# Kernel optimization log

Measured on AMD Instinct MI355X. Metric: run time of the kernel, lower is better.

Reference implementation:

```python
import jax, jax.numpy as jnp
import numpy as np

BH, BW = 4, 4  # bin_size_h, bin_size_w
BN_EPS = 1e-5


def _patch_split(t, bh, bw):
    # b c (bh ph) (bw pw) -> b (bh bw) (ph pw) c
    b, c, h, w = t.shape
    ph, pw = h // bh, w // bw
    t = t.reshape(b, c, bh, ph, bw, pw).transpose(0, 2, 4, 3, 5, 1)
    return t.reshape(b, bh * bw, ph * pw, c)


def _patch_recover(t, bh, bw, ph, pw):
    # b (bh bw) (ph pw) c -> b c (bh ph) (bw pw)
    b, n, p, c = t.shape
    t = t.reshape(b, bh, bw, ph, pw, c).transpose(0, 5, 1, 3, 2, 4)
    return t.reshape(b, c, bh * ph, bw * pw)


def setup_inputs() -> dict:
    key = jax.random.key(0)
    ks = jax.random.split(key, 16)
    b, C, h, w = 4, 512, 128, 128      # proj_dim = 512
    mid = C // 2                        # 256
    CM = 19 * 4                         # num_classes * num_local_prototype = 76
    return {
        "x": jax.random.normal(ks[0], (b, C, h, w), jnp.float32),
        "sim_mat": jax.random.normal(ks[1], (b, CM, h, w), jnp.float32),
        "global_cls_centers": jax.random.normal(ks[2], (19, 4, C), jnp.float32),
        "Wq": jax.random.normal(ks[3], (C, mid), jnp.float32) * 0.02,
        "bq": jax.random.normal(ks[4], (mid,), jnp.float32) * 0.02,
        "Wk": jax.random.normal(ks[5], (C, mid), jnp.float32) * 0.02,
        "bk": jax.random.normal(ks[6], (mid,), jnp.float32) * 0.02,
        "Wv": jax.random.normal(ks[7], (C, mid), jnp.float32) * 0.02,
        "bv": jax.random.normal(ks[8], (mid,), jnp.float32) * 0.02,
        "Wc": jax.random.normal(ks[9], (mid, C), jnp.float32) * 0.02,
        "bn_gamma": jax.random.uniform(ks[10], (C,), jnp.float32, 0.5, 1.5),
        "bn_beta": jax.random.normal(ks[11], (C,), jnp.float32) * 0.1,
        "bn_mean": jax.random.normal(ks[12], (C,), jnp.float32) * 0.1,
        "bn_var": jax.random.uniform(ks[13], (C,), jnp.float32, 0.5, 1.5),
    }


def reference(x, sim_mat, global_cls_centers, Wq, bq, Wk, bk, Wv, bv, Wc,
              bn_gamma, bn_beta, bn_mean, bn_var):
    b, C, h, w = x.shape
    CM = sim_mat.shape[1]
    ph, pw = h // BH, w // BW

    # pool_cam: adaptive avg pool to (BH, BW) == per-patch mean
    patch_cls_score = sim_mat.reshape(b, CM, BH, ph, BW, pw).mean(axis=(3, 5))  # [b,CM,BH,BW]

    sm = _patch_split(sim_mat, BH, BW)   # [b, N, P, CM]
    xs = _patch_split(x, BH, BW)         # [b, N, P, C]

    # patch_confidence: [b, N, CM, 1]
    conf = patch_cls_score.reshape(b, CM, BH * BW).transpose(0, 2, 1)[..., None]

    sm = jax.nn.softmax(sm, axis=2)      # softmax over pixels within patch
    local = jnp.einsum('bnpc,bnpk->bnck', sm, xs) * conf  # [b, N, CM, C]

    g = global_cls_centers.reshape(CM, C)  # (c m) k

    q = xs @ Wq + bq        # [b, N, P, mid]
    k = local @ Wk + bk     # [b, N, CM, mid]
    v = g @ Wv + bv         # [CM, mid] (identical across b, n -> broadcast)

    att = jax.nn.softmax(jnp.einsum('bnpm,bncm->bnpc', q, k), axis=-1)
    out = jnp.einsum('bnpc,cm->bnpm', att, v)               # [b, N, P, mid]

    out = _patch_recover(out, BH, BW, ph, pw)               # [b, mid, h, w]

    # conv_out: 1x1 conv (no bias) + BN (eval) + ReLU
    y = jnp.einsum('bmhw,mk->bkhw', out, Wc)
    inv = bn_gamma / jnp.sqrt(bn_var + BN_EPS)
    y = y * inv[None, :, None, None] + (bn_beta - bn_mean * inv)[None, :, None, None]
    y = jax.nn.relu(y)
    return (y, patch_cls_score)
```

## Files before the change

### kernel.cpp

```cpp
#include <hip/hip_runtime.h>

#define CM_    76
#define CMP_   80

typedef __attribute__((ext_vector_type(4))) float f32x4;
typedef __attribute__((ext_vector_type(8))) short bf16x8;

__device__ __forceinline__ unsigned short f2bf(float f) {
  union { float f; unsigned u; } v; v.f = f;
  unsigned r = v.u + 0x7FFFu + ((v.u >> 16) & 1u);
  return (unsigned short)(r >> 16);
}
__device__ __forceinline__ unsigned pack2(float a, float b) {
  return (unsigned)f2bf(a) | ((unsigned)f2bf(b) << 16);
}

#define OFF_BK2     0
#define OFF_INV     5120
#define OFF_ADD     5632
#define OFF_WKBQ    6144
#define OFF_BQKADD  6656
#define OFF_CBB     7168
#define OFF_EXPSIM  7172
#define OFF_LOCALBF 2628612
#define OFF_WQKT    3939332
#define OFF_VWT     5250052
#define OFF_WQWKT   5274628
#define OFF_WVWCT   5405700

__global__ __launch_bounds__(256) void kW_pre(
    const float* __restrict__ Wq, const float* __restrict__ Wk,
    const float* __restrict__ Wv, const float* __restrict__ Wc,
    const float* __restrict__ bq, const float* __restrict__ bk,
    const float* __restrict__ gamma, const float* __restrict__ beta,
    const float* __restrict__ mean, const float* __restrict__ var,
    unsigned short* __restrict__ WqWkT, unsigned short* __restrict__ WvWcT,
    float* __restrict__ wkbq, float* __restrict__ bqkadd,
    float* __restrict__ invp, float* __restrict__ addp, float* __restrict__ cbbp) {
  const int sel = blockIdx.y;
  if (blockIdx.x == 64) {
    const int c = sel * 256 + threadIdx.x;
    const float* wkr = Wk + (size_t)c * 256;
    const float* wqr = Wq + (size_t)c * 256;
    float s1 = 0.f, s2 = 0.f;
    for (int m = 0; m < 256; ++m) { s1 += wkr[m] * bq[m]; s2 += wqr[m] * bk[m]; }
    wkbq[c] = s1; bqkadd[c] = s2;
    float iv = gamma[c] * rsqrtf(var[c] + 1e-5f);
    invp[c] = iv; addp[c] = beta[c] - mean[c] * iv;
    if (c == 0) {
      float s = 0.f;
      for (int m = 0; m < 256; ++m) s += bq[m] * bk[m];
      cbbp[0] = s;
    }
    return;
  }
  const int r0 = (blockIdx.x >> 3) * 64, c0 = (blockIdx.x & 7) * 64;
  __shared__ __align__(16) unsigned short Asm[64 * 40];
  __shared__ __align__(16) unsigned short Bsm[64 * 40];
  const int t = threadIdx.x, lane = t & 63, w = t >> 6;
  const int lo = lane & 15, hi = lane >> 4;
  f32x4 acc[4];
#pragma unroll
  for (int cT = 0; cT < 4; ++cT) acc[cT] = (f32x4){0.f, 0.f, 0.f, 0.f};
  const float* Bsrc = sel ? Wv : Wk;
  for (int kc = 0; kc < 8; ++kc) {
    const int k0 = kc * 32;
    __syncthreads();
    {
      int nn = t >> 2, mq = (t & 3) * 8;
      const float* src = Bsrc + (size_t)(c0 + nn) * 256 + k0 + mq;
      float4 v0 = *(const float4*)src, v1 = *(const float4*)(src + 4);
      unsigned* d = (unsigned*)&Bsm[nn * 40 + mq];
      d[0] = pack2(v0.x, v0.y); d[1] = pack2(v0.z, v0.w);
      d[2] = pack2(v1.x, v1.y); d[3] = pack2(v1.z, v1.w);
    }
    if (sel == 0) {
      int r = t >> 2, mq = (t & 3) * 8;
      const float* src = Wq + (size_t)(r0 + r) * 256 + k0 + mq;
      float4 v0 = *(const float4*)src, v1 = *(const float4*)(src + 4);
      unsigned* d = (unsigned*)&Asm[r * 40 + mq];
      d[0] = pack2(v0.x, v0.y); d[1] = pack2(v0.z, v0.w);
      d[2] = pack2(v1.x, v1.y); d[3] = pack2(v1.z, v1.w);
    } else {
      int m = t >> 3, c2q = (t & 7) * 8;
      const float* src = Wc + (size_t)(k0 + m) * 512 + r0 + c2q;
      float4 v0 = *(const float4*)src, v1 = *(const float4*)(src + 4);
      Asm[(c2q + 0) * 40 + m] = f2bf(v0.x); Asm[(c2q + 1) * 40 + m] = f2bf(v0.y);
      Asm[(c2q + 2) * 40 + m] = f2bf(v0.z); Asm[(c2q + 3) * 40 + m] = f2bf(v0.w);
      Asm[(c2q + 4) * 40 + m] = f2bf(v1.x); Asm[(c2q + 5) * 40 + m] = f2bf(v1.y);
      Asm[(c2q + 6) * 40 + m] = f2bf(v1.z); Asm[(c2q + 7) * 40 + m] = f2bf(v1.w);
    }
    __syncthreads();
    bf16x8 afr = *(bf16x8*)(&Asm[(w * 16 + lo) * 40 + hi * 8]);
#pragma unroll
    for (int cT = 0; cT < 4; ++cT) {
      bf16x8 bfr = *(bf16x8*)(&Bsm[(cT * 16 + lo) * 40 + hi * 8]);
      acc[cT] = __builtin_amdgcn_mfma_f32_16x16x32_bf16(afr, bfr, acc[cT], 0, 0, 0);
    }
  }
  unsigned short* dst = sel ? WvWcT : WqWkT;
#pragma unroll
  for (int cT = 0; cT < 4; ++cT)
#pragma unroll
    for (int rr = 0; rr < 4; ++rr)
      dst[(size_t)(r0 + w * 16 + hi * 4 + rr) * 512 + c0 + cT * 16 + lo] = f2bf(acc[cT][rr]);
}

__global__ __launch_bounds__(256) void k1_stats(
    const float* __restrict__ sim, float* __restrict__ pcs,
    const float* __restrict__ cbbp,
    unsigned short* __restrict__ expsim, float* __restrict__ bk2) {
  const int cm = blockIdx.x, inst = blockIdx.y;
  const int t = threadIdx.x;
  unsigned short* erow = expsim + (size_t)inst * 81920 + (size_t)cm * 1024;
  if (cm >= CM_) {
    ((unsigned long long*)erow)[t] = 0ull;
    if (t == 0) bk2[inst * CMP_ + cm] = -1e30f;
    return;
  }
  const int b = inst >> 4, n = inst & 15, bh = n >> 2, bw = n & 3;
  const float* base = sim + ((size_t)(b * CM_ + cm) << 14);
  float v[4];
  float lsum = 0.f, lmax = -1e30f;
#pragma unroll
  for (int i = 0; i < 4; ++i) {
    int p = t + (i << 8);
    int pix = ((bh * 32 + (p >> 5)) << 7) + bw * 32 + (p & 31);
    float xv = base[pix];
    v[i] = xv; lsum += xv; lmax = fmaxf(lmax, xv);
  }
#pragma unroll
  for (int off = 32; off; off >>= 1) {
    lsum += __shfl_down(lsum, off);
    lmax = fmaxf(lmax, __shfl_down(lmax, off));
  }
  __shared__ float ssum[4], smax[4], bc[2];
  const int wid = t >> 6;
  if ((t & 63) == 0) { ssum[wid] = lsum; smax[wid] = lmax; }
  __syncthreads();
  if (t == 0) {
    bc[0] = ssum[0] + ssum[1] + ssum[2] + ssum[3];
    bc[1] = fmaxf(fmaxf(smax[0], smax[1]), fmaxf(smax[2], smax[3]));
  }
  __syncthreads();
  const float M = bc[1];
  float le = 0.f;
#pragma unroll
  for (int i = 0; i < 4; ++i) le += __expf(v[i] - M);
#pragma unroll
  for (int off = 32; off; off >>= 1) le += __shfl_down(le, off);
  if ((t & 63) == 0) ssum[wid] = le;
  __syncthreads();
  if (t == 0) {
    float E = ssum[0] + ssum[1] + ssum[2] + ssum[3];
    float conf = bc[0] * (1.f / 1024.f);
    pcs[((b * CM_ + cm) << 4) + n] = conf;
    bk2[inst * CMP_ + cm] = cbbp[0];
    bc[0] = conf / E;
  }
  __syncthreads();
  const float sc = bc[0];
#pragma unroll
  for (int i = 0; i < 4; ++i) {
    int p = t + (i << 8);
    erow[p] = f2bf(sc * __expf(v[i] - M));
  }
}

__global__ __launch_bounds__(256) void k2_local(
    const float* __restrict__ x, const unsigned short* __restrict__ expsim,
    const float* __restrict__ wkbq,
    unsigned short* __restrict__ local_bf, float* __restrict__ bk2) {
  const int cc = blockIdx.x, inst = blockIdx.y;
  const int b = inst >> 4, n = inst & 15, bh = n >> 2, bw = n & 3;
  const int t = threadIdx.x, lane = t & 63, w = t >> 6;
  const int lo = lane & 15, hi = lane >> 4;
  const int chw = cc * 64 + w * 16;
  const unsigned short* Abase = expsim + (size_t)inst * 81920;
  const float* xch = x + (((size_t)(b * 512 + chw + lo)) << 14) + bw * 32 + hi * 8;
  const int rowb = bh * 32;
  f32x4 acc[5];
#pragma unroll
  for (int T = 0; T < 5; ++T) acc[T] = (f32x4){0.f, 0.f, 0.f, 0.f};
#pragma unroll 4
  for (int ks = 0; ks < 32; ++ks) {
    const int k = ks * 32 + hi * 8;
    const float* xr = xch + ((size_t)(rowb + ks) << 7);
    float4 v0 = *(const float4*)(xr);
    float4 v1 = *(const float4*)(xr + 4);
    bf16x8 bfr;
    ((unsigned*)&bfr)[0] = pack2(v0.x, v0.y);
    ((unsigned*)&bfr)[1] = pack2(v0.z, v0.w);
    ((unsigned*)&bfr)[2] = pack2(v1.x, v1.y);
    ((unsigned*)&bfr)[3] = pack2(v1.z, v1.w);
#pragma unroll
    for (int T = 0; T < 5; ++T) {
      bf16x8 afr = *(const bf16x8*)(Abase + (size_t)(T * 16 + lo) * 1024 + k);
      acc[T] = __builtin_amdgcn_mfma_f32_16x16x32_bf16(afr, bfr, acc[T], 0, 0, 0);
    }
  }
  const float wk = wkbq[chw + lo];
#pragma unroll
  for (int T = 0; T < 5; ++T)
#pragma unroll
    for (int r = 0; r < 4; ++r) {
      int cm = T * 16 + hi * 4 + r;
      float av = acc[T][r];
      local_bf[((size_t)inst * CMP_ + cm) * 512 + chw + lo] = f2bf(av);
      float p = av * wk;
      p += __shfl_xor(p, 1); p += __shfl_xor(p, 2);
      p += __shfl_xor(p, 4); p += __shfl_xor(p, 8);
      if (lo == 0 && cm < CM_) atomicAdd(&bk2[inst * CMP_ + cm], p);
    }
}

__global__ __launch_bounds__(256) void k3n_wqkt(
    const unsigned short* __restrict__ local_bf, const unsigned short* __restrict__ WqWkT,
    const float* __restrict__ bqkadd, unsigned short* __restrict__ Wqkt) {
  const int blkc = blockIdx.x, inst = blockIdx.y;
  const int t = threadIdx.x, lane = t & 63, w = t >> 6;
  const int lo = lane & 15, hi = lane >> 4;
  const int cbase = blkc * 128 + w * 32;
  f32x4 acc[5][2];
#pragma unroll
  for (int cT = 0; cT < 2; ++cT) {
    float bv_ = bqkadd[cbase + cT * 16 + lo];
#pragma unroll
    for (int T = 0; T < 5; ++T) acc[T][cT] = (f32x4){bv_, bv_, bv_, bv_};
  }
  const unsigned short* Abase = local_bf + (size_t)inst * 40960;
#pragma unroll 4
  for (int ks = 0; ks < 16; ++ks) {
    const int k = ks * 32 + hi * 8;
    bf16x8 af[5];
#pragma unroll
    for (int T = 0; T < 5; ++T)
      af[T] = *(const bf16x8*)(Abase + (size_t)(T * 16 + lo) * 512 + k);
#pragma unroll
    for (int cT = 0; cT < 2; ++cT) {
      bf16x8 bfr = *(const bf16x8*)(WqWkT + (size_t)(cbase + cT * 16 + lo) * 512 + k);
#pragma unroll
      for (int T = 0; T < 5; ++T)
        acc[T][cT] = __builtin_amdgcn_mfma_f32_16x16x32_bf16(af[T], bfr, acc[T][cT], 0, 0, 0);
    }
  }
#pragma unroll
  for (int T = 0; T < 5; ++T)
#pragma unroll
    for (int cT = 0; cT < 2; ++cT)
#pragma unroll
      for (int r = 0; r < 4; ++r) {
        int cm = T * 16 + hi * 4 + r;
        Wqkt[(size_t)inst * 40960 + (size_t)cm * 512 + cbase + cT * 16 + lo] =
            f2bf(acc[T][cT][r]);
      }
}

__global__ __launch_bounds__(256) void kV_vwt(
    const unsigned short* __restrict__ WvWcT, const float* __restrict__ g,
    const float* __restrict__ bv, const float* __restrict__ Wc,
    unsigned short* __restrict__ vWt) {
  const int blk = blockIdx.x, half = blockIdx.y;
  const int t = threadIdx.x, lane = t & 63, w = t >> 6;
  const int lo = lane & 15, hi = lane >> 4;
  __shared__ float bvp[4][64];
  __shared__ float bvs[64];
  {
    int c2l = t & 63, part = t >> 6;
    float s = 0.f;
    for (int m = part * 64; m < part * 64 + 64; ++m)
      s += bv[m] * Wc[(size_t)m * 512 + blk * 64 + c2l];
    bvp[part][c2l] = s;
  }
  __syncthreads();
  if (t < 64) bvs[t] = bvp[0][t] + bvp[1][t] + bvp[2][t] + bvp[3][t];
  __syncthreads();
  const int r2 = blk * 64 + w * 16;
  f32x4 acc[3];
#pragma unroll
  for (int j = 0; j < 3; ++j) acc[j] = (f32x4){0.f, 0.f, 0.f, 0.f};
#pragma unroll 4
  for (int ks = 0; ks < 16; ++ks) {
    const int k = ks * 32 + hi * 8;
    bf16x8 afr = *(const bf16x8*)(WvWcT + (size_t)(r2 + lo) * 512 + k);
#pragma unroll
    for (int j = 0; j < 3; ++j) {
      int cm = (half * 3 + j) * 16 + lo;
      cm = cm > 75 ? 75 : cm;
      const float* gr = g + (size_t)cm * 512 + k;
      float4 v0 = *(const float4*)gr, v1 = *(const float4*)(gr + 4);
      bf16x8 bfr;
      ((unsigned*)&bfr)[0] = pack2(v0.x, v0.y);
      ((unsigned*)&bfr)[1] = pack2(v0.z, v0.w);
      ((unsigned*)&bfr)[2] = pack2(v1.x, v1.y);
      ((unsigned*)&bfr)[3] = pack2(v1.z, v1.w);
      acc[j] = __builtin_amdgcn_mfma_f32_16x16x32_bf16(afr, bfr, acc[j], 0, 0, 0);
    }
  }
#pragma unroll
  for (int j = 0; j < 3; ++j)
#pragma unroll
    for (int rr = 0; rr < 4; ++rr) {
      int c2g = blk * 64 + w * 16 + hi * 4 + rr;
      vWt[(size_t)c2g * 96 + (half * 3 + j) * 16 + lo] =
          f2bf(acc[j][rr] + bvs[w * 16 + hi * 4 + rr]);
    }
}

__global__ __launch_bounds__(256) void k4_attn(
    const float* __restrict__ x, const unsigned short* __restrict__ Wqkt,
    const float* __restrict__ bk2, const unsigned short* __restrict__ vWt,
    const float* __restrict__ inv_arr, const float* __restrict__ add_arr,
    float* __restrict__ y) {
  const int pt = blockIdx.x, inst = blockIdx.y;
  const int b = inst >> 4, n = inst & 15, bh = n >> 2, bw = n & 3;
  __shared__ unsigned short Xs[4][32 * 72];
  __shared__ unsigned short Att[4][32 * 96];
  __shared__ float bn_s[1024];
  const int t = threadIdx.x, lane = t & 63, w = t >> 6;
  const int lo = lane & 15, hi = lane >> 4;
  const int pq = lane & 7, chp0 = lane >> 3;

  for (int i = t; i < 512; i += 256) { bn_s[i] = inv_arr[i]; bn_s[512 + i] = add_arr[i]; }

  const int imgrow = bh * 32 + pt * 4 + w;
  const size_t pixbase = (size_t)imgrow * 128 + bw * 32;
  const size_t xrowbase = (((size_t)b * 512) << 14) + pixbase;
  const unsigned short* Wi = Wqkt + (size_t)inst * 40960;

  f32x4 acc[2][5];
#pragma unroll
  for (int T = 0; T < 5; ++T) {
    f32x4 bv;
#pragma unroll
    for (int r = 0; r < 4; ++r) bv[r] = bk2[inst * CMP_ + T * 16 + hi * 4 + r];
    acc[0][T] = bv; acc[1][T] = bv;
  }

  for (int kc = 0; kc < 8; ++kc) {
#pragma unroll
    for (int i = 0; i < 4; ++i) {
      int chp = chp0 + i * 8;
      int ch = kc * 64 + chp * 2;
      const float* xa = x + xrowbase + ((size_t)ch << 14) + pq * 4;
      float4 va = *(const float4*)(xa);
      float4 vb = *(const float4*)(xa + 16384);
      unsigned short* dst = &Xs[w][(pq * 4) * 72 + chp * 2];
      *(unsigned*)(dst + 0 * 72) = pack2(va.x, vb.x);
      *(unsigned*)(dst + 1 * 72) = pack2(va.y, vb.y);
      *(unsigned*)(dst + 2 * 72) = pack2(va.z, vb.z);
      *(unsigned*)(dst + 3 * 72) = pack2(va.w, vb.w);
    }
#pragma unroll
    for (int ks = 0; ks < 2; ++ks) {
      int kb = kc * 64 + ks * 32 + hi * 8;
      bf16x8 b0 = *(bf16x8*)(&Xs[w][lo * 72 + ks * 32 + hi * 8]);
      bf16x8 b1 = *(bf16x8*)(&Xs[w][(16 + lo) * 72 + ks * 32 + hi * 8]);
#pragma unroll
      for (int T = 0; T < 5; ++T) {
        bf16x8 afr = *(const bf16x8*)(Wi + (size_t)(T * 16 + lo) * 512 + kb);
        acc[0][T] = __builtin_amdgcn_mfma_f32_16x16x32_bf16(afr, b0, acc[0][T], 0, 0, 0);
        acc[1][T] = __builtin_amdgcn_mfma_f32_16x16x32_bf16(afr, b1, acc[1][T], 0, 0, 0);
      }
    }
  }

#pragma unroll
  for (int p = 0; p < 2; ++p) {
    float m = -1e30f;
#pragma unroll
    for (int T = 0; T < 5; ++T)
#pragma unroll
      for (int r = 0; r < 4; ++r) m = fmaxf(m, acc[p][T][r]);
    m = fmaxf(m, __shfl_xor(m, 16));
    m = fmaxf(m, __shfl_xor(m, 32));
    float e[5][4];
    float s = 0.f;
#pragma unroll
    for (int T = 0; T < 5; ++T)
#pragma unroll
      for (int r = 0; r < 4; ++r) { float ev = __expf(acc[p][T][r] - m); e[T][r] = ev; s += ev; }
    s += __shfl_xor(s, 16);
    s += __shfl_xor(s, 32);
    float rinv = 1.f / s;
    int px = p * 16 + lo;
#pragma unroll
    for (int T = 0; T < 5; ++T) {
      unsigned l32 = pack2(e[T][0] * rinv, e[T][1] * rinv);
      unsigned h32 = pack2(e[T][2] * rinv, e[T][3] * rinv);
      *(unsigned long long*)(&Att[w][px * 96 + T * 16 + hi * 4]) =
          (unsigned long long)l32 | ((unsigned long long)h32 << 32);
    }
    *(unsigned long long*)(&Att[w][px * 96 + 80 + hi * 4]) = 0ull;
  }

  __syncthreads();

  bf16x8 bfr3[2][3];
#pragma unroll
  for (int p = 0; p < 2; ++p)
#pragma unroll
    for (int ks = 0; ks < 3; ++ks)
      bfr3[p][ks] = *(bf16x8*)(&Att[w][(p * 16 + lo) * 96 + ks * 32 + hi * 8]);

  for (int cT = 0; cT < 32; ++cT) {
    f32x4 a0 = (f32x4){0.f, 0.f, 0.f, 0.f}, a1 = a0;
    const unsigned short* vr = vWt + (size_t)(cT * 16 + lo) * 96;
#pragma unroll
    for (int ks = 0; ks < 3; ++ks) {
      bf16x8 afr = *(const bf16x8*)(vr + ks * 32 + hi * 8);
      a0 = __builtin_amdgcn_mfma_f32_16x16x32_bf16(afr, bfr3[0][ks], a0, 0, 0, 0);
      a1 = __builtin_amdgcn_mfma_f32_16x16x32_bf16(afr, bfr3[1][ks], a1, 0, 0, 0);
    }
    f32x4 inv4 = *(f32x4*)(&bn_s[cT * 16 + hi * 4]);
    f32x4 add4 = *(f32x4*)(&bn_s[512 + cT * 16 + hi * 4]);
#pragma unroll
    for (int r = 0; r < 4; ++r) {
      int ch = cT * 16 + hi * 4 + r;
      float v0 = fmaxf(a0[r] * inv4[r] + add4[r], 0.f);
      float v1 = fmaxf(a1[r] * inv4[r] + add4[r], 0.f);
      size_t yb = (((size_t)(b * 512 + ch)) << 14) + pixbase;
      y[yb + lo] = v0;
      y[yb + 16 + lo] = v1;
    }
  }
}

extern "C" void kernel_launch(void* const* d_in, const int* in_sizes, int n_in,
                              void* d_out, int out_size, void* d_ws, size_t ws_size,
                              hipStream_t stream) {
  (void)in_sizes; (void)n_in; (void)out_size; (void)ws_size;
  const float* x     = (const float*)d_in[0];
  const float* sim   = (const float*)d_in[1];
  const float* g     = (const float*)d_in[2];
  const float* Wq    = (const float*)d_in[3];
  const float* bq    = (const float*)d_in[4];
  const float* Wk    = (const float*)d_in[5];
  const float* bk    = (const float*)d_in[6];
  const float* Wv    = (const float*)d_in[7];
  const float* bv    = (const float*)d_in[8];
  const float* Wc    = (const float*)d_in[9];
  const float* gamma = (const float*)d_in[10];
  const float* beta  = (const float*)d_in[11];
  const float* mean  = (const float*)d_in[12];
  const float* var   = (const float*)d_in[13];
  float* out = (float*)d_out;
  float* ws  = (float*)d_ws;
  float* y   = out;
  float* pcs = out + 33554432;
  unsigned short* expsim  = (unsigned short*)(ws + OFF_EXPSIM);
  unsigned short* localbf = (unsigned short*)(ws + OFF_LOCALBF);
  unsigned short* Wqkt    = (unsigned short*)(ws + OFF_WQKT);
  unsigned short* vWt     = (unsigned short*)(ws + OFF_VWT);
  unsigned short* WqWkT   = (unsigned short*)(ws + OFF_WQWKT);
  unsigned short* WvWcT   = (unsigned short*)(ws + OFF_WVWCT);

  hipLaunchKernelGGL(kW_pre, dim3(65, 2), dim3(256), 0, stream,
                     Wq, Wk, Wv, Wc, bq, bk, gamma, beta, mean, var,
                     WqWkT, WvWcT, ws + OFF_WKBQ, ws + OFF_BQKADD,
                     ws + OFF_INV, ws + OFF_ADD, ws + OFF_CBB);
  hipLaunchKernelGGL(k1_stats, dim3(CMP_, 64), dim3(256), 0, stream,
                     sim, pcs, ws + OFF_CBB, expsim, ws + OFF_BK2);
  hipLaunchKernelGGL(k2_local, dim3(8, 64), dim3(256), 0, stream,
                     x, expsim, ws + OFF_WKBQ, localbf, ws + OFF_BK2);
  hipLaunchKernelGGL(k3n_wqkt, dim3(4, 64), dim3(256), 0, stream,
                     localbf, WqWkT, ws + OFF_BQKADD, Wqkt);
  hipLaunchKernelGGL(kV_vwt, dim3(8, 2), dim3(256), 0, stream,
                     WvWcT, g, bv, Wc, vWt);
  hipLaunchKernelGGL(k4_attn, dim3(8, 64), dim3(256), 0, stream,
                     x, Wqkt, ws + OFF_BK2, vWt,
                     ws + OFF_INV, ws + OFF_ADD, y);
}
```

Baseline: 424.8 us.

## Split K across waves and raise grid sizes in local, wqkt and attention kernels

k1 now loads four contiguous pixels per thread as a float4 and writes packed bf16. k2 splits the 1024-pixel reduction across the four waves and combines the partial sums through shared memory, using 4x more blocks. k3 halves the channel tile per block and doubles the grid. k4 splits the q·k reduction over channels between wave pairs and reduces through shared memory, and splits the output channels across waves with twice the blocks. The aim is more parallelism and occupancy on underfilled grids, at the cost of extra shared-memory traffic, extra syncs and more redundant operand loads.

```diff
diff --git a/kernel.cpp b/kernel.cpp
--- a/kernel.cpp
+++ b/kernel.cpp
@@ -120,15 +120,11 @@
   }
   const int b = inst >> 4, n = inst & 15, bh = n >> 2, bw = n & 3;
   const float* base = sim + ((size_t)(b * CM_ + cm) << 14);
-  float v[4];
-  float lsum = 0.f, lmax = -1e30f;
-#pragma unroll
-  for (int i = 0; i < 4; ++i) {
-    int p = t + (i << 8);
-    int pix = ((bh * 32 + (p >> 5)) << 7) + bw * 32 + (p & 31);
-    float xv = base[pix];
-    v[i] = xv; lsum += xv; lmax = fmaxf(lmax, xv);
-  }
+  const int p0 = t * 4;
+  const int pix0 = ((bh * 32 + (p0 >> 5)) << 7) + bw * 32 + (p0 & 31);
+  float4 vv = *(const float4*)(base + pix0);
+  float lsum = vv.x + vv.y + vv.z + vv.w;
+  float lmax = fmaxf(fmaxf(vv.x, vv.y), fmaxf(vv.z, vv.w));
 #pragma unroll
   for (int off = 32; off; off >>= 1) {
     lsum += __shfl_down(lsum, off);
@@ -144,9 +140,9 @@
   }
   __syncthreads();
   const float M = bc[1];
-  float le = 0.f;
-#pragma unroll
-  for (int i = 0; i < 4; ++i) le += __expf(v[i] - M);
+  float e0 = __expf(vv.x - M), e1 = __expf(vv.y - M);
+  float e2 = __expf(vv.z - M), e3 = __expf(vv.w - M);
+  float le = (e0 + e1) + (e2 + e3);
 #pragma unroll
   for (int off = 32; off; off >>= 1) le += __shfl_down(le, off);
   if ((t & 63) == 0) ssum[wid] = le;
@@ -160,31 +156,30 @@
   }
   __syncthreads();
   const float sc = bc[0];
-#pragma unroll
-  for (int i = 0; i < 4; ++i) {
-    int p = t + (i << 8);
-    erow[p] = f2bf(sc * __expf(v[i] - M));
-  }
+  unsigned l32 = pack2(sc * e0, sc * e1);
+  unsigned h32 = pack2(sc * e2, sc * e3);
+  *(unsigned long long*)(&erow[p0]) = (unsigned long long)l32 | ((unsigned long long)h32 << 32);
 }
 
 __global__ __launch_bounds__(256) void k2_local(
     const float* __restrict__ x, const unsigned short* __restrict__ expsim,
     const float* __restrict__ wkbq,
     unsigned short* __restrict__ local_bf, float* __restrict__ bk2) {
-  const int cc = blockIdx.x, inst = blockIdx.y;
+  const int ccc = blockIdx.x, inst = blockIdx.y;
   const int b = inst >> 4, n = inst & 15, bh = n >> 2, bw = n & 3;
   const int t = threadIdx.x, lane = t & 63, w = t >> 6;
   const int lo = lane & 15, hi = lane >> 4;
-  const int chw = cc * 64 + w * 16;
+  const int ch0 = ccc * 16;
+  __shared__ float Red[4 * 80 * 17];
   const unsigned short* Abase = expsim + (size_t)inst * 81920;
-  const float* xch = x + (((size_t)(b * 512 + chw + lo)) << 14) + bw * 32 + hi * 8;
-  const int rowb = bh * 32;
+  const float* xch = x + (((size_t)(b * 512 + ch0 + lo)) << 14) + bw * 32 + hi * 8;
+  const int rowb = bh * 32 + w * 8;
   f32x4 acc[5];
 #pragma unroll
   for (int T = 0; T < 5; ++T) acc[T] = (f32x4){0.f, 0.f, 0.f, 0.f};
-#pragma unroll 4
-  for (int ks = 0; ks < 32; ++ks) {
-    const int k = ks * 32 + hi * 8;
+#pragma unroll
+  for (int ks = 0; ks < 8; ++ks) {
+    const int k = w * 256 + ks * 32 + hi * 8;
     const float* xr = xch + ((size_t)(rowb + ks) << 7);
     float4 v0 = *(const float4*)(xr);
     float4 v1 = *(const float4*)(xr + 4);
@@ -199,19 +194,25 @@
       acc[T] = __builtin_amdgcn_mfma_f32_16x16x32_bf16(afr, bfr, acc[T], 0, 0, 0);
     }
   }
-  const float wk = wkbq[chw + lo];
 #pragma unroll
   for (int T = 0; T < 5; ++T)
 #pragma unroll
-    for (int r = 0; r < 4; ++r) {
-      int cm = T * 16 + hi * 4 + r;
-      float av = acc[T][r];
-      local_bf[((size_t)inst * CMP_ + cm) * 512 + chw + lo] = f2bf(av);
-      float p = av * wk;
-      p += __shfl_xor(p, 1); p += __shfl_xor(p, 2);
-      p += __shfl_xor(p, 4); p += __shfl_xor(p, 8);
-      if (lo == 0 && cm < CM_) atomicAdd(&bk2[inst * CMP_ + cm], p);
-    }
+    for (int r = 0; r < 4; ++r)
+      Red[w * 1360 + (T * 16 + hi * 4 + r) * 17 + lo] = acc[T][r];
+  __syncthreads();
+  const int ch = t & 15, cmg = t >> 4;
+  const float wk = wkbq[ch0 + ch];
+#pragma unroll
+  for (int j = 0; j < 5; ++j) {
+    int cm = cmg + 16 * j;
+    float av = Red[cm * 17 + ch] + Red[1360 + cm * 17 + ch] +
+               Red[2720 + cm * 17 + ch] + Red[4080 + cm * 17 + ch];
+    local_bf[((size_t)inst * CMP_ + cm) * 512 + ch0 + ch] = f2bf(av);
+    float p = av * wk;
+    p += __shfl_xor(p, 1); p += __shfl_xor(p, 2);
+    p += __shfl_xor(p, 4); p += __shfl_xor(p, 8);
+    if (ch == 0 && cm < CM_) atomicAdd(&bk2[inst * CMP_ + cm], p);
+  }
 }
 
 __global__ __launch_bounds__(256) void k3n_wqkt(
@@ -220,40 +221,31 @@
   const int blkc = blockIdx.x, inst = blockIdx.y;
   const int t = threadIdx.x, lane = t & 63, w = t >> 6;
   const int lo = lane & 15, hi = lane >> 4;
-  const int cbase = blkc * 128 + w * 32;
-  f32x4 acc[5][2];
-#pragma unroll
-  for (int cT = 0; cT < 2; ++cT) {
-    float bv_ = bqkadd[cbase + cT * 16 + lo];
-#pragma unroll
-    for (int T = 0; T < 5; ++T) acc[T][cT] = (f32x4){bv_, bv_, bv_, bv_};
+  const int cbase = blkc * 64 + w * 16;
+  f32x4 acc[5];
+  {
+    float bv_ = bqkadd[cbase + lo];
+#pragma unroll
+    for (int T = 0; T < 5; ++T) acc[T] = (f32x4){bv_, bv_, bv_, bv_};
   }
   const unsigned short* Abase = local_bf + (size_t)inst * 40960;
 #pragma unroll 4
   for (int ks = 0; ks < 16; ++ks) {
     const int k = ks * 32 + hi * 8;
-    bf16x8 af[5];
-#pragma unroll
-    for (int T = 0; T < 5; ++T)
-      af[T] = *(const bf16x8*)(Abase + (size_t)(T * 16 + lo) * 512 + k);
-#pragma unroll
-    for (int cT = 0; cT < 2; ++cT) {
-      bf16x8 bfr = *(const bf16x8*)(WqWkT + (size_t)(cbase + cT * 16 + lo) * 512 + k);
-#pragma unroll
-      for (int T = 0; T < 5; ++T)
-        acc[T][cT] = __builtin_amdgcn_mfma_f32_16x16x32_bf16(af[T], bfr, acc[T][cT], 0, 0, 0);
+    bf16x8 bfr = *(const bf16x8*)(WqWkT + (size_t)(cbase + lo) * 512 + k);
+#pragma unroll
+    for (int T = 0; T < 5; ++T) {
+      bf16x8 af = *(const bf16x8*)(Abase + (size_t)(T * 16 + lo) * 512 + k);
+      acc[T] = __builtin_amdgcn_mfma_f32_16x16x32_bf16(af, bfr, acc[T], 0, 0, 0);
     }
   }
 #pragma unroll
   for (int T = 0; T < 5; ++T)
 #pragma unroll
-    for (int cT = 0; cT < 2; ++cT)
-#pragma unroll
-      for (int r = 0; r < 4; ++r) {
-        int cm = T * 16 + hi * 4 + r;
-        Wqkt[(size_t)inst * 40960 + (size_t)cm * 512 + cbase + cT * 16 + lo] =
-            f2bf(acc[T][cT][r]);
-      }
+    for (int r = 0; r < 4; ++r) {
+      int cm = T * 16 + hi * 4 + r;
+      Wqkt[(size_t)inst * 40960 + (size_t)cm * 512 + cbase + lo] = f2bf(acc[T][r]);
+    }
 }
 
 __global__ __launch_bounds__(256) void kV_vwt(
@@ -312,32 +304,41 @@
     const float* __restrict__ bk2, const unsigned short* __restrict__ vWt,
     const float* __restrict__ inv_arr, const float* __restrict__ add_arr,
     float* __restrict__ y) {
-  const int pt = blockIdx.x, inst = blockIdx.y;
+  const int pt2 = blockIdx.x, inst = blockIdx.y;
   const int b = inst >> 4, n = inst & 15, bh = n >> 2, bw = n & 3;
-  __shared__ unsigned short Xs[4][32 * 72];
-  __shared__ unsigned short Att[4][32 * 96];
-  __shared__ float bn_s[1024];
+  __shared__ __align__(16) char Ubuf[20736];
+  __shared__ unsigned short Att[2][32 * 96];
+  unsigned short* Xs = (unsigned short*)Ubuf;
+  float* Red = (float*)Ubuf;
   const int t = threadIdx.x, lane = t & 63, w = t >> 6;
   const int lo = lane & 15, hi = lane >> 4;
   const int pq = lane & 7, chp0 = lane >> 3;
-
-  for (int i = t; i < 512; i += 256) { bn_s[i] = inv_arr[i]; bn_s[512 + i] = add_arr[i]; }
-
-  const int imgrow = bh * 32 + pt * 4 + w;
+  const int r = w & 1, h = w >> 1;
+
+  const int imgrow = bh * 32 + pt2 * 2 + r;
   const size_t pixbase = (size_t)imgrow * 128 + bw * 32;
   const size_t xrowbase = (((size_t)b * 512) << 14) + pixbase;
   const unsigned short* Wi = Wqkt + (size_t)inst * 40960;
 
   f32x4 acc[2][5];
-#pragma unroll
-  for (int T = 0; T < 5; ++T) {
-    f32x4 bv;
-#pragma unroll
-    for (int r = 0; r < 4; ++r) bv[r] = bk2[inst * CMP_ + T * 16 + hi * 4 + r];
-    acc[0][T] = bv; acc[1][T] = bv;
-  }
-
-  for (int kc = 0; kc < 8; ++kc) {
+  if (h == 0) {
+#pragma unroll
+    for (int T = 0; T < 5; ++T) {
+      f32x4 bv;
+#pragma unroll
+      for (int r4 = 0; r4 < 4; ++r4) bv[r4] = bk2[inst * CMP_ + T * 16 + hi * 4 + r4];
+      acc[0][T] = bv; acc[1][T] = bv;
+    }
+  } else {
+#pragma unroll
+    for (int T = 0; T < 5; ++T) {
+      acc[0][T] = (f32x4){0.f, 0.f, 0.f, 0.f};
+      acc[1][T] = (f32x4){0.f, 0.f, 0.f, 0.f};
+    }
+  }
+#pragma unroll
+  for (int kci = 0; kci < 4; ++kci) {
+    const int kc = h * 4 + kci;
 #pragma unroll
     for (int i = 0; i < 4; ++i) {
       int chp = chp0 + i * 8;
@@ -345,7 +346,7 @@
       const float* xa = x + xrowbase + ((size_t)ch << 14) + pq * 4;
       float4 va = *(const float4*)(xa);
       float4 vb = *(const float4*)(xa + 16384);
-      unsigned short* dst = &Xs[w][(pq * 4) * 72 + chp * 2];
+      unsigned short* dst = &Xs[w * 2304 + (pq * 4) * 72 + chp * 2];
       *(unsigned*)(dst + 0 * 72) = pack2(va.x, vb.x);
       *(unsigned*)(dst + 1 * 72) = pack2(va.y, vb.y);
       *(unsigned*)(dst + 2 * 72) = pack2(va.z, vb.z);
@@ -354,8 +355,8 @@
 #pragma unroll
     for (int ks = 0; ks < 2; ++ks) {
       int kb = kc * 64 + ks * 32 + hi * 8;
-      bf16x8 b0 = *(bf16x8*)(&Xs[w][lo * 72 + ks * 32 + hi * 8]);
-      bf16x8 b1 = *(bf16x8*)(&Xs[w][(16 + lo) * 72 + ks * 32 + hi * 8]);
+      bf16x8 b0 = *(bf16x8*)(&Xs[w * 2304 + lo * 72 + ks * 32 + hi * 8]);
+      bf16x8 b1 = *(bf16x8*)(&Xs[w * 2304 + (16 + lo) * 72 + ks * 32 + hi * 8]);
 #pragma unroll
       for (int T = 0; T < 5; ++T) {
         bf16x8 afr = *(const bf16x8*)(Wi + (size_t)(T * 16 + lo) * 512 + kb);
@@ -364,46 +365,66 @@
       }
     }
   }
-
-#pragma unroll
-  for (int p = 0; p < 2; ++p) {
-    float m = -1e30f;
-#pragma unroll
-    for (int T = 0; T < 5; ++T)
-#pragma unroll
-      for (int r = 0; r < 4; ++r) m = fmaxf(m, acc[p][T][r]);
-    m = fmaxf(m, __shfl_xor(m, 16));
-    m = fmaxf(m, __shfl_xor(m, 32));
-    float e[5][4];
-    float s = 0.f;
-#pragma unroll
-    for (int T = 0; T < 5; ++T)
-#pragma unroll
-      for (int r = 0; r < 4; ++r) { float ev = __expf(acc[p][T][r] - m); e[T][r] = ev; s += ev; }
-    s += __shfl_xor(s, 16);
-    s += __shfl_xor(s, 32);
-    float rinv = 1.f / s;
-    int px = p * 16 + lo;
-#pragma unroll
-    for (int T = 0; T < 5; ++T) {
-      unsigned l32 = pack2(e[T][0] * rinv, e[T][1] * rinv);
-      unsigned h32 = pack2(e[T][2] * rinv, e[T][3] * rinv);
-      *(unsigned long long*)(&Att[w][px * 96 + T * 16 + hi * 4]) =
-          (unsigned long long)l32 | ((unsigned long long)h32 << 32);
-    }
-    *(unsigned long long*)(&Att[w][px * 96 + 80 + hi * 4]) = 0ull;
-  }
-
-  __syncthreads();
-
+  __syncthreads();
+  if (h == 1) {
+#pragma unroll
+    for (int p = 0; p < 2; ++p)
+#pragma unroll
+      for (int T = 0; T < 5; ++T)
+#pragma unroll
+        for (int r4 = 0; r4 < 4; ++r4)
+          Red[r * 2592 + (p * 16 + lo) * 81 + T * 16 + hi * 4 + r4] = acc[p][T][r4];
+  }
+  __syncthreads();
+  if (h == 0) {
+#pragma unroll
+    for (int p = 0; p < 2; ++p) {
+#pragma unroll
+      for (int T = 0; T < 5; ++T)
+#pragma unroll
+        for (int r4 = 0; r4 < 4; ++r4)
+          acc[p][T][r4] += Red[r * 2592 + (p * 16 + lo) * 81 + T * 16 + hi * 4 + r4];
+      float m = -1e30f;
+#pragma unroll
+      for (int T = 0; T < 5; ++T)
+#pragma unroll
+        for (int r4 = 0; r4 < 4; ++r4) m = fmaxf(m, acc[p][T][r4]);
+      m = fmaxf(m, __shfl_xor(m, 16));
+      m = fmaxf(m, __shfl_xor(m, 32));
+      float e[5][4];
+      float s = 0.f;
+#pragma unroll
+      for (int T = 0; T < 5; ++T)
+#pragma unroll
+        for (int r4 = 0; r4 < 4; ++r4) {
+          float ev = __expf(acc[p][T][r4] - m); e[T][r4] = ev; s += ev;
+        }
+      s += __shfl_xor(s, 16);
+      s += __shfl_xor(s, 32);
+      float rinv = 1.f / s;
+      int px = p * 16 + lo;
+#pragma unroll
+      for (int T = 0; T < 5; ++T) {
+        unsigned l32 = pack2(e[T][0] * rinv, e[T][1] * rinv);
+        unsigned h32 = pack2(e[T][2] * rinv, e[T][3] * rinv);
+        *(unsigned long long*)(&Att[r][px * 96 + T * 16 + hi * 4]) =
+            (unsigned long long)l32 | ((unsigned long long)h32 << 32);
+      }
+      *(unsigned long long*)(&Att[r][px * 96 + 80 + hi * 4]) = 0ull;
+    }
+  }
+  __syncthreads();
+
+  const int rr = w & 1, cgrp = w >> 1;
+  const size_t pixb3 = (size_t)(bh * 32 + pt2 * 2 + rr) * 128 + bw * 32;
   bf16x8 bfr3[2][3];
 #pragma unroll
   for (int p = 0; p < 2; ++p)
 #pragma unroll
     for (int ks = 0; ks < 3; ++ks)
-      bfr3[p][ks] = *(bf16x8*)(&Att[w][(p * 16 + lo) * 96 + ks * 32 + hi * 8]);
-
-  for (int cT = 0; cT < 32; ++cT) {
+      bfr3[p][ks] = *(bf16x8*)(&Att[rr][(p * 16 + lo) * 96 + ks * 32 + hi * 8]);
+
+  for (int cT = cgrp * 16; cT < cgrp * 16 + 16; ++cT) {
     f32x4 a0 = (f32x4){0.f, 0.f, 0.f, 0.f}, a1 = a0;
     const unsigned short* vr = vWt + (size_t)(cT * 16 + lo) * 96;
 #pragma unroll
@@ -412,14 +433,14 @@
       a0 = __builtin_amdgcn_mfma_f32_16x16x32_bf16(afr, bfr3[0][ks], a0, 0, 0, 0);
       a1 = __builtin_amdgcn_mfma_f32_16x16x32_bf16(afr, bfr3[1][ks], a1, 0, 0, 0);
     }
-    f32x4 inv4 = *(f32x4*)(&bn_s[cT * 16 + hi * 4]);
-    f32x4 add4 = *(f32x4*)(&bn_s[512 + cT * 16 + hi * 4]);
-#pragma unroll
-    for (int r = 0; r < 4; ++r) {
-      int ch = cT * 16 + hi * 4 + r;
-      float v0 = fmaxf(a0[r] * inv4[r] + add4[r], 0.f);
-      float v1 = fmaxf(a1[r] * inv4[r] + add4[r], 0.f);
-      size_t yb = (((size_t)(b * 512 + ch)) << 14) + pixbase;
+    f32x4 inv4 = *(const f32x4*)(inv_arr + cT * 16 + hi * 4);
+    f32x4 add4 = *(const f32x4*)(add_arr + cT * 16 + hi * 4);
+#pragma unroll
+    for (int r4 = 0; r4 < 4; ++r4) {
+      int ch = cT * 16 + hi * 4 + r4;
+      float v0 = fmaxf(a0[r4] * inv4[r4] + add4[r4], 0.f);
+      float v1 = fmaxf(a1[r4] * inv4[r4] + add4[r4], 0.f);
+      size_t yb = (((size_t)(b * 512 + ch)) << 14) + pixb3;
       y[yb + lo] = v0;
       y[yb + 16 + lo] = v1;
     }
@@ -461,13 +482,13 @@
                      ws + OFF_INV, ws + OFF_ADD, ws + OFF_CBB);
   hipLaunchKernelGGL(k1_stats, dim3(CMP_, 64), dim3(256), 0, stream,
                      sim, pcs, ws + OFF_CBB, expsim, ws + OFF_BK2);
-  hipLaunchKernelGGL(k2_local, dim3(8, 64), dim3(256), 0, stream,
+  hipLaunchKernelGGL(k2_local, dim3(32, 64), dim3(256), 0, stream,
                      x, expsim, ws + OFF_WKBQ, localbf, ws + OFF_BK2);
-  hipLaunchKernelGGL(k3n_wqkt, dim3(4, 64), dim3(256), 0, stream,
+  hipLaunchKernelGGL(k3n_wqkt, dim3(8, 64), dim3(256), 0, stream,
                      localbf, WqWkT, ws + OFF_BQKADD, Wqkt);
   hipLaunchKernelGGL(kV_vwt, dim3(8, 2), dim3(256), 0, stream,
                      WvWcT, g, bv, Wc, vWt);
-  hipLaunchKernelGGL(k4_attn, dim3(8, 64), dim3(256), 0, stream,
+  hipLaunchKernelGGL(k4_attn, dim3(16, 64), dim3(256), 0, stream,
                      x, Wqkt, ws + OFF_BK2, vWt,
                      ws + OFF_INV, ws + OFF_ADD, y);
 }
```

New measurement: 476.2 us. 12.1% more time.
